# Optimization experiments

Hardware: AMD Instinct MI355X
Metric: run time of the kernel (lower is better)

Reference implementation:

```python
import jax, jax.numpy as jnp
import numpy as np

N_NODES = 10000
N_EDGES = 160000
MUL_N = 64    # node-feature multiplicity per irrep (0e and 1o)
MUL_F = 16    # field-feature multiplicity per irrep
SQ3 = np.sqrt(3.0).astype(np.float32)
SILU_GAIN = np.float32(1.679177)  # e3nn normalize2mom gain for silu


def split_irreps(x, mul):
    # x: [n, mul + 3*mul] laid out e3nn-style: scalars then vectors
    return x[:, :mul], x[:, mul:].reshape(x.shape[0], mul, 3)


def irrep_linear(s, v, Ws, Wv):
    # o3.Linear on (mul x0e + mul x1o): per-irrep channel mixing, 1/sqrt(fan_in)
    inv = np.float32(1.0 / np.sqrt(Ws.shape[0]))
    return (s @ Ws) * inv, jnp.einsum('nui,uv->nvi', v, Wv) * inv


def setup_inputs() -> dict:
    key = jax.random.key(0)
    ks = jax.random.split(key, 30)
    f32 = jnp.float32
    rn = lambda k, sh: jax.random.normal(k, sh, dtype=f32)
    inp = {
        'node_attrs': rn(ks[0], (N_NODES, 10)),
        'node_feats': rn(ks[1], (N_NODES, MUL_N + 3 * MUL_N)),
        'edge_attrs': rn(ks[2], (N_EDGES, 4)),
        'edge_feats': rn(ks[3], (N_EDGES, 8)),
        'field_feats': rn(ks[4], (N_NODES, MUL_F + 3 * MUL_F)),
        'edge_index': jax.random.randint(ks[5], (2, N_EDGES), 0, N_NODES, dtype=jnp.int32),
        # o3.Linear weights (linear1, linear2)
        'W1s': rn(ks[6], (MUL_N, MUL_N)), 'W1v': rn(ks[7], (MUL_N, MUL_N)),
        'W2s': rn(ks[8], (MUL_N, MUL_N)), 'W2v': rn(ks[9], (MUL_N, MUL_N)),
        # FullyConnectedNet [8,64,64,64,256]
        'mlp_w1': rn(ks[10], (8, 64)), 'mlp_w2': rn(ks[11], (64, 64)),
        'mlp_w3': rn(ks[12], (64, 64)), 'mlp_w4': rn(ks[13], (64, 4 * MUL_N)),
        # linear_v_sender / linear_v_receiver: 128x0e+128x1o -> 16x0e+16x1o
        'Wvs_s': rn(ks[14], (2 * MUL_N, MUL_F)), 'Wvs_v': rn(ks[15], (2 * MUL_N, MUL_F)),
        'Wvr_s': rn(ks[16], (2 * MUL_N, MUL_F)), 'Wvr_v': rn(ks[17], (2 * MUL_N, MUL_F)),
        # final FC tensor products (field x field -> 1x0e)
        'Wfs0': rn(ks[18], (MUL_F, MUL_F)), 'Wfs1': rn(ks[19], (MUL_F, MUL_F)),
        'Wfr0': rn(ks[20], (MUL_F, MUL_F)), 'Wfr1': rn(ks[21], (MUL_F, MUL_F)),
        # LinearInFieldChargesBlock FC TP: node x field -> 1x0e+1x1o
        'Wmp_ss': rn(ks[22], (MUL_N, MUL_F)), 'Wmp_vv': rn(ks[23], (MUL_N, MUL_F)),
        'Wmp_sv': rn(ks[24], (MUL_N, MUL_F)), 'Wmp_vs': rn(ks[25], (MUL_N, MUL_F)),
    }
    return inp


def reference(node_attrs, node_feats, edge_attrs, edge_feats, field_feats,
              W1s, W1v, W2s, W2v, mlp_w1, mlp_w2, mlp_w3, mlp_w4,
              Wvs_s, Wvs_v, Wvr_s, Wvr_v, Wfs0, Wfs1, Wfr0, Wfr1,
              Wmp_ss, Wmp_vv, Wmp_sv, Wmp_vs, edge_index):
    sender, receiver = edge_index[0], edge_index[1]
    num_nodes = node_feats.shape[0]

    # conv_tp weight MLP (e3nn FullyConnectedNet)
    h = edge_feats
    for W in (mlp_w1, mlp_w2, mlp_w3):
        h = jax.nn.silu((h @ W) * np.float32(1.0 / np.sqrt(W.shape[0]))) * SILU_GAIN
    tp_w = (h @ mlp_w4) * np.float32(1.0 / np.sqrt(mlp_w4.shape[0]))  # [E, 4*MUL_N]
    w = tp_w.reshape(-1, 4, MUL_N)

    ns, nv = split_irreps(node_feats, MUL_N)
    l1s, l1v = irrep_linear(ns, nv, W1s, W1v)
    l2s, l2v = irrep_linear(ns, nv, W2s, W2v)
    bs = l1s[sender] + l2s[receiver]   # [E, MUL_N]
    bv = l1v[sender] + l2v[receiver]   # [E, MUL_N, 3]

    y0 = edge_attrs[:, 0:1]            # [E,1] 0e harmonic
    y1 = edge_attrs[:, 1:4]            # [E,3] 1o harmonic
    # uvu CG tensor product with per-edge weights
    m00 = w[:, 0] * bs * y0                                          # 0e x 0e -> 0e
    m11 = w[:, 1] * jnp.einsum('eui,ei->eu', bv, y1) / SQ3           # 1o x 1o -> 0e
    m01 = w[:, 2][:, :, None] * bs[:, :, None] * y1[:, None, :]      # 0e x 1o -> 1o
    m10 = w[:, 3][:, :, None] * bv * y0[:, :, None]                  # 1o x 0e -> 1o
    ms = jnp.concatenate([m00, m11], axis=1)    # [E, 128]
    mv = jnp.concatenate([m01, m10], axis=1)    # [E, 128, 3]

    As, Av = irrep_linear(ms, mv, Wvs_s, Wvs_v)
    Bs, Bv = irrep_linear(ms, mv, Wvr_s, Wvr_v)

    fs, fv = split_irreps(field_feats, MUL_F)
    alpha = np.float32(1.0 / np.sqrt(2 * MUL_F * MUL_F))
    p_s = (jnp.einsum('eu,ev,uv->e', As, fs[sender], Wfs0)
           + jnp.einsum('eui,evi,uv->e', Av, fv[sender], Wfs1) / SQ3) * alpha
    p_r = (jnp.einsum('eu,ev,uv->e', Bs, fs[receiver], Wfr0)
           + jnp.einsum('eui,evi,uv->e', Bv, fv[receiver], Wfr1) / SQ3) * alpha
    p_ji = np.float32(0.1) * (p_s + p_r)   # [E]

    charges = (jax.ops.segment_sum(p_ji, receiver, num_segments=num_nodes)
               - jax.ops.segment_sum(p_ji, sender, num_segments=num_nodes))

    # field-dependent multipoles (FC TP, zero_charges=True then charge slot overwritten)
    a2 = np.float32(1.0 / np.sqrt(2 * MUL_N * MUL_F))
    mp0 = (jnp.einsum('nu,nv,uv->n', ns, fs, Wmp_ss)
           + jnp.einsum('nui,nvi,uv->n', nv, fv, Wmp_vv) / SQ3) * a2
    mp1 = (jnp.einsum('nu,nvi,uv->ni', ns, fv, Wmp_sv)
           + jnp.einsum('nui,nv,uv->ni', nv, fs, Wmp_vs)) * a2
    mpoles = np.float32(0.01) * jnp.concatenate([mp0[:, None], mp1], axis=1)  # [N,4]
    mpoles = mpoles.at[:, 0].set(charges)
    return mpoles[:, None, :], p_ji[:, None]
```

## Files before the change

### kernel.cpp

```cpp
#include <hip/hip_runtime.h>

#define NN 10000
#define NE 160000

#define INV8   0.35355339059327373f
#define QINV   0.125f
#define GAIN   1.679177f
#define ISQ3   0.57735026918962576f
#define FINALS 4.8828125e-5f
#define MPSC   2.2097086912079612e-4f

typedef __attribute__((ext_vector_type(8))) short bf16x8;
typedef __attribute__((ext_vector_type(4))) float f32x4;

__device__ __forceinline__ float4 ld4(const float* p){ return *(const float4*)p; }
__device__ __forceinline__ float sil(float x){ return x*GAIN/(1.f+__expf(-x)); }
__device__ __forceinline__ unsigned short f2b(float f){
  unsigned u = __float_as_uint(f);
  return (unsigned short)((u + 0x7FFFu + ((u>>16)&1u)) >> 16);
}
__device__ __forceinline__ float b2f(unsigned short b){
  return __uint_as_float(((unsigned)b) << 16);
}
__device__ __forceinline__ void st4b(unsigned short* p, float a, float b, float c, float d){
  unsigned long long v = (unsigned long long)f2b(a)
                       | ((unsigned long long)f2b(b) << 16)
                       | ((unsigned long long)f2b(c) << 32)
                       | ((unsigned long long)f2b(d) << 48);
  *(unsigned long long*)p = v;
}
__device__ __forceinline__ void up8(const unsigned short* p, float* f){
  const uint4 v = *(const uint4*)p;
  f[0]=__uint_as_float(v.x<<16); f[1]=__uint_as_float(v.x&0xFFFF0000u);
  f[2]=__uint_as_float(v.y<<16); f[3]=__uint_as_float(v.y&0xFFFF0000u);
  f[4]=__uint_as_float(v.z<<16); f[5]=__uint_as_float(v.z&0xFFFF0000u);
  f[6]=__uint_as_float(v.w<<16); f[7]=__uint_as_float(v.w&0xFFFF0000u);
}
#define C4(v,i) (((const float*)&(v))[i])

#define WQ_STRIDE 260
__global__ __launch_bounds__(256, 2) void edge_fused_kernel(
    const float* __restrict__ efe,
    const float* __restrict__ mw1, const float* __restrict__ mw2,
    const float* __restrict__ mw3, const float* __restrict__ mw4,
    const float* __restrict__ ea, const int* __restrict__ eidx,
    const unsigned short* __restrict__ wsS, const unsigned short* __restrict__ wsR,
    float* __restrict__ out)
{
  __shared__ __align__(16) unsigned char pool[8192 + 128*WQ_STRIDE*2];
  unsigned short* W4q = (unsigned short*)pool;
  unsigned short* W1t = (unsigned short*)(pool + 8192);
  unsigned short* W2t = (unsigned short*)(pool + 12288);
  unsigned short* W3t = (unsigned short*)(pool + 20480);
  unsigned short* H   = (unsigned short*)(pool + 28672);
  unsigned short* WQ  = (unsigned short*)(pool + 8192);

  const int tid = threadIdx.x;
  const int wv  = tid >> 6;
  const int l   = tid & 63;
  const int eb  = blockIdx.x * 128;

  #pragma unroll
  for (int it = 0; it < 16; ++it) {
    const int i = tid + 256*it, e = i >> 5, k = i & 31;
    H[e*64 + (k ^ ((e&7)<<3))] = (k < 8) ? f2b(efe[(size_t)(eb+e)*8 + k]) : 0;
  }
  #pragma unroll
  for (int it = 0; it < 8; ++it) {
    const int i = tid + 256*it, n = i >> 5, k = i & 31;
    W1t[n*32 + (k ^ ((n&3)<<3))] = (k < 8) ? f2b(mw1[k*64 + n]) : 0;
  }
  #pragma unroll
  for (int it = 0; it < 16; ++it) {
    const int i = tid + 256*it, k = i >> 6, n = i & 63;
    W2t[n*64 + (k ^ ((n&7)<<3))] = f2b(mw2[k*64 + n]);
    W3t[n*64 + (k ^ ((n&7)<<3))] = f2b(mw3[k*64 + n]);
  }
  __syncthreads();

  const int arow = l & 15;
  const int koff = (l >> 4) * 8;

  {
    bf16x8 a[8];
    #pragma unroll
    for (int mf = 0; mf < 8; ++mf) {
      const int e = mf*16 + arow;
      a[mf] = *(const bf16x8*)&H[e*64 + (koff ^ ((e&7)<<3))];
    }
    const int n = wv*16 + arow;
    const bf16x8 b = *(const bf16x8*)&W1t[n*32 + (koff ^ ((n&3)<<3))];
    __syncthreads();
    f32x4 acc[8];
    #pragma unroll
    for (int mf = 0; mf < 8; ++mf) {
      acc[mf] = (f32x4){0.f,0.f,0.f,0.f};
      acc[mf] = __builtin_amdgcn_mfma_f32_16x16x32_bf16(a[mf], b, acc[mf], 0, 0, 0);
    }
    #pragma unroll
    for (int mf = 0; mf < 8; ++mf)
      #pragma unroll
      for (int rg = 0; rg < 4; ++rg) {
        const int e = mf*16 + (l>>4)*4 + rg, j = wv*16 + arow;
        H[e*64 + (j ^ ((e&7)<<3))] = f2b(sil(acc[mf][rg]*INV8));
      }
    __syncthreads();
  }

  const unsigned short* Wt[2] = { W2t, W3t };
  #pragma unroll
  for (int ly = 0; ly < 2; ++ly) {
    bf16x8 a[16];
    #pragma unroll
    for (int mf = 0; mf < 8; ++mf)
      #pragma unroll
      for (int ks = 0; ks < 2; ++ks) {
        const int e = mf*16 + arow, kb = ks*32 + koff;
        a[mf*2+ks] = *(const bf16x8*)&H[e*64 + (kb ^ ((e&7)<<3))];
      }
    const int n = wv*16 + arow;
    bf16x8 b0, b1;
    {
      const int kb0 = koff, kb1 = 32 + koff;
      b0 = *(const bf16x8*)&Wt[ly][n*64 + (kb0 ^ ((n&7)<<3))];
      b1 = *(const bf16x8*)&Wt[ly][n*64 + (kb1 ^ ((n&7)<<3))];
    }
    __syncthreads();
    f32x4 acc[8];
    #pragma unroll
    for (int mf = 0; mf < 8; ++mf) {
      acc[mf] = (f32x4){0.f,0.f,0.f,0.f};
      acc[mf] = __builtin_amdgcn_mfma_f32_16x16x32_bf16(a[mf*2+0], b0, acc[mf], 0, 0, 0);
      acc[mf] = __builtin_amdgcn_mfma_f32_16x16x32_bf16(a[mf*2+1], b1, acc[mf], 0, 0, 0);
    }
    #pragma unroll
    for (int mf = 0; mf < 8; ++mf)
      #pragma unroll
      for (int rg = 0; rg < 4; ++rg) {
        const int e = mf*16 + (l>>4)*4 + rg, j = wv*16 + arow;
        H[e*64 + (j ^ ((e&7)<<3))] = f2b(sil(acc[mf][rg]*QINV));
      }
    __syncthreads();
  }

  bf16x8 a4[16];
  #pragma unroll
  for (int mf = 0; mf < 8; ++mf)
    #pragma unroll
    for (int ks = 0; ks < 2; ++ks) {
      const int e = mf*16 + arow, kb = ks*32 + koff;
      a4[mf*2+ks] = *(const bf16x8*)&H[e*64 + (kb ^ ((e&7)<<3))];
    }

  for (int q = 0; q < 4; ++q) {
    #pragma unroll
    for (int it = 0; it < 16; ++it) {
      const int i = tid + 256*it, k = i >> 6, nn = i & 63;
      W4q[nn*64 + (k ^ ((nn&7)<<3))] = f2b(mw4[k*256 + q*64 + nn]);
    }
    __syncthreads();

    const int n = wv*16 + arow;
    const bf16x8 b0 = *(const bf16x8*)&W4q[n*64 + ((koff     ) ^ ((n&7)<<3))];
    const bf16x8 b1 = *(const bf16x8*)&W4q[n*64 + ((32 + koff) ^ ((n&7)<<3))];
    f32x4 acc[8];
    #pragma unroll
    for (int mf = 0; mf < 8; ++mf) {
      acc[mf] = (f32x4){0.f,0.f,0.f,0.f};
      acc[mf] = __builtin_amdgcn_mfma_f32_16x16x32_bf16(a4[mf*2+0], b0, acc[mf], 0, 0, 0);
      acc[mf] = __builtin_amdgcn_mfma_f32_16x16x32_bf16(a4[mf*2+1], b1, acc[mf], 0, 0, 0);
    }
    #pragma unroll
    for (int mf = 0; mf < 8; ++mf)
      #pragma unroll
      for (int rg = 0; rg < 4; ++rg) {
        const int e = mf*16 + (l>>4)*4 + rg;
        const int j = q*64 + wv*16 + arow;
        WQ[e*WQ_STRIDE + j] = f2b(acc[mf][rg]);
      }
    __syncthreads();
  }

  {
    const int el  = tid >> 1;
    const int sub = tid & 1;
    const int e   = eb + el;
    const int s = eidx[e];
    const int r = eidx[NE + e];
    const float4 y = ld4(ea + (size_t)e*4);

    float accS = 0.f, accR = 0.f;
    const unsigned short* Sb = wsS + (size_t)s*768 + sub*384;
    const unsigned short* Rb = wsR + (size_t)r*768 + sub*384;
    const unsigned short* wrow = WQ + el*WQ_STRIDE;
    #pragma unroll 2
    for (int t = 0; t < 8; ++t) {
      const int uq = sub*8 + t;
      const unsigned short* Sr = Sb + t*48;
      const unsigned short* Rr = Rb + t*48;
      float S[48], R[48];
      up8(Sr+ 0, S+ 0); up8(Sr+ 8, S+ 8); up8(Sr+16, S+16);
      up8(Sr+24, S+24); up8(Sr+32, S+32); up8(Sr+40, S+40);
      up8(Rr+ 0, R+ 0); up8(Rr+ 8, R+ 8); up8(Rr+16, R+16);
      up8(Rr+24, R+24); up8(Rr+32, R+32); up8(Rr+40, R+40);

      float wq[16];
      #pragma unroll
      for (int m = 0; m < 4; ++m) {
        const unsigned long long v = *(const unsigned long long*)(wrow + m*64 + uq*4);
        #pragma unroll
        for (int d = 0; d < 4; ++d)
          wq[m*4+d] = b2f((unsigned short)(v >> (16*d)));
      }

      #pragma unroll
      for (int d = 0; d < 4; ++d) {
        const float bs = S[d]    + R[d];
        const float b0 = S[4+d]  + R[4+d];
        const float b1 = S[8+d]  + R[8+d];
        const float b2 = S[12+d] + R[12+d];
        const float bvy = b0*y.y + b1*y.z + b2*y.w;
        const float m0 = wq[d]    * bs * y.x;
        const float m1 = wq[4+d]  * bvy;
        const float m2 = wq[8+d]  * bs;
        const float m3 = wq[12+d] * y.x;
        accS += m0*S[16+d] + m1*S[20+d]
              + m2*(y.y*S[24+d] + y.z*S[28+d] + y.w*S[32+d])
              + m3*(b0*S[36+d] + b1*S[40+d] + b2*S[44+d]);
        accR += m0*R[16+d] + m1*R[20+d]
              + m2*(y.y*R[24+d] + y.z*R[28+d] + y.w*R[32+d])
              + m3*(b0*R[36+d] + b1*R[40+d] + b2*R[44+d]);
      }
    }
    float acc = FINALS * (accS + accR);
    acc += __shfl_xor(acc, 1, 64);
    if (sub == 0) {
      out[NN*4 + e] = acc;
      atomicAdd(out + (size_t)r*4, acc);
      atomicAdd(out + (size_t)s*4, -acc);
    }
  }
}

__global__ __launch_bounds__(256) void node_kernel(
    const float* __restrict__ nf, const float* __restrict__ ff,
    const float* __restrict__ W1s, const float* __restrict__ W1v,
    const float* __restrict__ W2s, const float* __restrict__ W2v,
    const float* __restrict__ Wvss, const float* __restrict__ Wvsv,
    const float* __restrict__ Wvrs, const float* __restrict__ Wvrv,
    const float* __restrict__ Wfs0, const float* __restrict__ Wfs1,
    const float* __restrict__ Wfr0, const float* __restrict__ Wfr1,
    const float* __restrict__ Wmsv, const float* __restrict__ Wmvs,
    unsigned short* __restrict__ wsS, unsigned short* __restrict__ wsR,
    float* __restrict__ out)
{
  const int lane = threadIdx.x & 63;
  const int Wid  = blockIdx.x * 4 + (threadIdx.x >> 6);
  const int p    = __builtin_amdgcn_readfirstlane(Wid & 7);
  const int grp  = __builtin_amdgcn_readfirstlane(Wid >> 3);
  const int n = grp * 64 + lane;
  if (n >= NN) return;
  const float* nrow = nf + (size_t)n * 256;
  const int vb = p * 8;
  const size_t rec = (size_t)n * 768;

  float a1s[8], a2s[8], a1v[3][8], a2v[3][8], t1[16];
  #pragma unroll
  for (int j = 0; j < 8; ++j){ a1s[j]=0.f; a2s[j]=0.f;
    a1v[0][j]=0.f; a1v[1][j]=0.f; a1v[2][j]=0.f;
    a2v[0][j]=0.f; a2v[1][j]=0.f; a2v[2][j]=0.f; }
  #pragma unroll
  for (int j = 0; j < 16; ++j) t1[j]=0.f;

  for (int u = 0; u < 64; ++u) {
    const float su  = nrow[u];
    const float nv0 = nrow[64+u*3+0];
    const float nv1 = nrow[64+u*3+1];
    const float nv2 = nrow[64+u*3+2];
    const float4 s1a = ld4(W1s+u*64+vb), s1b = ld4(W1s+u*64+vb+4);
    const float4 s2a = ld4(W2s+u*64+vb), s2b = ld4(W2s+u*64+vb+4);
    const float4 v1a = ld4(W1v+u*64+vb), v1b = ld4(W1v+u*64+vb+4);
    const float4 v2a = ld4(W2v+u*64+vb), v2b = ld4(W2v+u*64+vb+4);
    #pragma unroll
    for (int d = 0; d < 4; ++d) {
      a1s[d]     += su*C4(s1a,d);  a1s[4+d]     += su*C4(s1b,d);
      a2s[d]     += su*C4(s2a,d);  a2s[4+d]     += su*C4(s2b,d);
      a1v[0][d]  += nv0*C4(v1a,d); a1v[0][4+d]  += nv0*C4(v1b,d);
      a1v[1][d]  += nv1*C4(v1a,d); a1v[1][4+d]  += nv1*C4(v1b,d);
      a1v[2][d]  += nv2*C4(v1a,d); a1v[2][4+d]  += nv2*C4(v1b,d);
      a2v[0][d]  += nv0*C4(v2a,d); a2v[0][4+d]  += nv0*C4(v2b,d);
      a2v[1][d]  += nv1*C4(v2a,d); a2v[1][4+d]  += nv1*C4(v2b,d);
      a2v[2][d]  += nv2*C4(v2a,d); a2v[2][4+d]  += nv2*C4(v2b,d);
    }
    if (p == 0) {
      #pragma unroll
      for (int q = 0; q < 4; ++q) {
        const float4 m = ld4(Wmsv + u*16 + q*4);
        t1[q*4]   += su*m.x; t1[q*4+1] += su*m.y;
        t1[q*4+2] += su*m.z; t1[q*4+3] += su*m.w;
      }
    }
  }
  #pragma unroll
  for (int hh = 0; hh < 2; ++hh) {
    const int uq = 2*p + hh, o = hh*4;
    unsigned short* S = wsS + rec + uq*48;
    unsigned short* R = wsR + rec + uq*48;
    st4b(S+0,  a1s[o]*QINV, a1s[o+1]*QINV, a1s[o+2]*QINV, a1s[o+3]*QINV);
    st4b(S+4,  a1v[0][o]*QINV, a1v[0][o+1]*QINV, a1v[0][o+2]*QINV, a1v[0][o+3]*QINV);
    st4b(S+8,  a1v[1][o]*QINV, a1v[1][o+1]*QINV, a1v[1][o+2]*QINV, a1v[1][o+3]*QINV);
    st4b(S+12, a1v[2][o]*QINV, a1v[2][o+1]*QINV, a1v[2][o+2]*QINV, a1v[2][o+3]*QINV);
    st4b(R+0,  a2s[o]*QINV, a2s[o+1]*QINV, a2s[o+2]*QINV, a2s[o+3]*QINV);
    st4b(R+4,  a2v[0][o]*QINV, a2v[0][o+1]*QINV, a2v[0][o+2]*QINV, a2v[0][o+3]*QINV);
    st4b(R+8,  a2v[1][o]*QINV, a2v[1][o+1]*QINV, a2v[1][o+2]*QINV, a2v[1][o+3]*QINV);
    st4b(R+12, a2v[2][o]*QINV, a2v[2][o+1]*QINV, a2v[2][o+2]*QINV, a2v[2][o+3]*QINV);
  }

  float fsv[16], fvv[48];
  {
    const float* fr = ff + (size_t)n*64;
    #pragma unroll
    for (int q = 0; q < 4; ++q) {
      const float4 t = ld4(fr + q*4);
      fsv[q*4]=t.x; fsv[q*4+1]=t.y; fsv[q*4+2]=t.z; fsv[q*4+3]=t.w;
    }
    #pragma unroll
    for (int q = 0; q < 12; ++q) {
      const float4 t = ld4(fr + 16 + q*4);
      fvv[q*4]=t.x; fvv[q*4+1]=t.y; fvv[q*4+2]=t.z; fvv[q*4+3]=t.w;
    }
  }

  if (p == 0) {
    float m0=0.f, m1=0.f, m2=0.f;
    #pragma unroll
    for (int v = 0; v < 16; ++v) {
      m0 += t1[v]*fvv[v*3]; m1 += t1[v]*fvv[v*3+1]; m2 += t1[v]*fvv[v*3+2];
    }
    for (int u = 0; u < 64; ++u) {
      float t2 = 0.f;
      #pragma unroll
      for (int q = 0; q < 4; ++q) {
        const float4 w = ld4(Wmvs + u*16 + q*4);
        t2 += w.x*fsv[q*4] + w.y*fsv[q*4+1] + w.z*fsv[q*4+2] + w.w*fsv[q*4+3];
      }
      m0 += nrow[64+u*3+0]*t2;
      m1 += nrow[64+u*3+1]*t2;
      m2 += nrow[64+u*3+2]*t2;
    }
    float* o = out + (size_t)n*4;
    o[0] = 0.f;
    o[1] = MPSC*m0; o[2] = MPSC*m1; o[3] = MPSC*m2;
  }

  float gsA[16], gsB[16], gvA[48], gvB[48];
  #pragma unroll
  for (int up = 0; up < 16; ++up) {
    float sA=0.f,sB=0.f,vA0=0.f,vA1=0.f,vA2=0.f,vB0=0.f,vB1=0.f,vB2=0.f;
    #pragma unroll
    for (int q = 0; q < 4; ++q) {
      const float4 w0 = ld4(Wfs0 + up*16 + q*4);
      const float4 w1 = ld4(Wfs1 + up*16 + q*4);
      const float4 w2 = ld4(Wfr0 + up*16 + q*4);
      const float4 w3 = ld4(Wfr1 + up*16 + q*4);
      #pragma unroll
      for (int d = 0; d < 4; ++d) {
        const int v = q*4+d;
        sA  += C4(w0,d)*fsv[v];
        sB  += C4(w2,d)*fsv[v];
        vA0 += C4(w1,d)*fvv[v*3]; vA1 += C4(w1,d)*fvv[v*3+1]; vA2 += C4(w1,d)*fvv[v*3+2];
        vB0 += C4(w3,d)*fvv[v*3]; vB1 += C4(w3,d)*fvv[v*3+1]; vB2 += C4(w3,d)*fvv[v*3+2];
      }
    }
    gsA[up]=sA; gsB[up]=sB;
    gvA[up*3]=vA0; gvA[up*3+1]=vA1; gvA[up*3+2]=vA2;
    gvB[up*3]=vB0; gvB[up*3+1]=vB1; gvB[up*3+2]=vB2;
  }

  #pragma unroll
  for (int tq = 0; tq < 4; ++tq) {
    float qa[4], qb[4], ra[3][4], rb[3][4];
    #pragma unroll
    for (int d = 0; d < 4; ++d) {
      const int U = p*16 + tq*4 + d;
      float aq=0.f,bq=0.f,a0=0.f,a1=0.f,a2=0.f,b0=0.f,b1=0.f,b2=0.f;
      #pragma unroll
      for (int q = 0; q < 4; ++q) {
        const float4 ws_ = ld4(Wvss + U*16 + q*4);
        const float4 wr_ = ld4(Wvrs + U*16 + q*4);
        const float4 wv_ = ld4(Wvsv + U*16 + q*4);
        const float4 wu_ = ld4(Wvrv + U*16 + q*4);
        #pragma unroll
        for (int dd = 0; dd < 4; ++dd) {
          const int up = q*4+dd;
          aq += C4(ws_,dd)*gsA[up];
          bq += C4(wr_,dd)*gsB[up];
          a0 += C4(wv_,dd)*gvA[up*3]; a1 += C4(wv_,dd)*gvA[up*3+1]; a2 += C4(wv_,dd)*gvA[up*3+2];
          b0 += C4(wu_,dd)*gvB[up*3]; b1 += C4(wu_,dd)*gvB[up*3+1]; b2 += C4(wu_,dd)*gvB[up*3+2];
        }
      }
      qa[d]=aq; qb[d]=bq;
      ra[0][d]=a0*ISQ3; ra[1][d]=a1*ISQ3; ra[2][d]=a2*ISQ3;
      rb[0][d]=b0*ISQ3; rb[1][d]=b1*ISQ3; rb[2][d]=b2*ISQ3;
    }
    if (p < 4) {
      const int uq = p*4 + tq;
      unsigned short* S = wsS + rec + uq*48;
      unsigned short* R = wsR + rec + uq*48;
      st4b(S+16, qa[0],qa[1],qa[2],qa[3]);
      st4b(S+24, ra[0][0],ra[0][1],ra[0][2],ra[0][3]);
      st4b(S+28, ra[1][0],ra[1][1],ra[1][2],ra[1][3]);
      st4b(S+32, ra[2][0],ra[2][1],ra[2][2],ra[2][3]);
      st4b(R+16, qb[0],qb[1],qb[2],qb[3]);
      st4b(R+24, rb[0][0],rb[0][1],rb[0][2],rb[0][3]);
      st4b(R+28, rb[1][0],rb[1][1],rb[1][2],rb[1][3]);
      st4b(R+32, rb[2][0],rb[2][1],rb[2][2],rb[2][3]);
    } else {
      const int uq = (p-4)*4 + tq;
      unsigned short* S = wsS + rec + uq*48;
      unsigned short* R = wsR + rec + uq*48;
      st4b(S+20, qa[0]*ISQ3,qa[1]*ISQ3,qa[2]*ISQ3,qa[3]*ISQ3);
      st4b(S+36, ra[0][0],ra[0][1],ra[0][2],ra[0][3]);
      st4b(S+40, ra[1][0],ra[1][1],ra[1][2],ra[1][3]);
      st4b(S+44, ra[2][0],ra[2][1],ra[2][2],ra[2][3]);
      st4b(R+20, qb[0]*ISQ3,qb[1]*ISQ3,qb[2]*ISQ3,qb[3]*ISQ3);
      st4b(R+36, rb[0][0],rb[0][1],rb[0][2],rb[0][3]);
      st4b(R+40, rb[1][0],rb[1][1],rb[1][2],rb[1][3]);
      st4b(R+44, rb[2][0],rb[2][1],rb[2][2],rb[2][3]);
    }
  }
}

extern "C" void kernel_launch(void* const* d_in, const int* in_sizes, int n_in,
                              void* d_out, int out_size, void* d_ws, size_t ws_size,
                              hipStream_t stream) {
  (void)in_sizes; (void)n_in; (void)out_size; (void)ws_size;
  const float* node_feats  = (const float*)d_in[1];
  const float* edge_attrs  = (const float*)d_in[2];
  const float* edge_feats  = (const float*)d_in[3];
  const float* field_feats = (const float*)d_in[4];
  const int*   edge_index  = (const int*)  d_in[5];
  const float* W1s  = (const float*)d_in[6];
  const float* W1v  = (const float*)d_in[7];
  const float* W2s  = (const float*)d_in[8];
  const float* W2v  = (const float*)d_in[9];
  const float* mw1  = (const float*)d_in[10];
  const float* mw2  = (const float*)d_in[11];
  const float* mw3  = (const float*)d_in[12];
  const float* mw4  = (const float*)d_in[13];
  const float* Wvss = (const float*)d_in[14];
  const float* Wvsv = (const float*)d_in[15];
  const float* Wvrs = (const float*)d_in[16];
  const float* Wvrv = (const float*)d_in[17];
  const float* Wfs0 = (const float*)d_in[18];
  const float* Wfs1 = (const float*)d_in[19];
  const float* Wfr0 = (const float*)d_in[20];
  const float* Wfr1 = (const float*)d_in[21];
  const float* Wmsv = (const float*)d_in[24];
  const float* Wmvs = (const float*)d_in[25];

  float* out = (float*)d_out;
  unsigned short* wsS = (unsigned short*)d_ws;
  unsigned short* wsR = wsS + (size_t)NN*768;

  hipLaunchKernelGGL(node_kernel, dim3(314), dim3(256), 0, stream,
      node_feats, field_feats, W1s, W1v, W2s, W2v, Wvss, Wvsv, Wvrs, Wvrv,
      Wfs0, Wfs1, Wfr0, Wfr1, Wmsv, Wmvs, wsS, wsR, out);
  hipLaunchKernelGGL(edge_fused_kernel, dim3(NE/128), dim3(256), 0, stream,
      edge_feats, mw1, mw2, mw3, mw4, edge_attrs, edge_index, wsS, wsR, out);
}
```

Measured before the change: 215.9 us.

## Sort edges by receiver via counting sort before the fused edge kernel

```diff
diff --git a/kernel.cpp b/kernel.cpp
--- a/kernel.cpp
+++ b/kernel.cpp
@@ -38,12 +38,66 @@
 }
 #define C4(v,i) (((const float*)&(v))[i])
 
+__global__ __launch_bounds__(256) void sort_zero(unsigned* __restrict__ hist){
+  hist[blockIdx.x*256 + threadIdx.x] = 0u;
+}
+__global__ __launch_bounds__(256) void sort_hist(const int* __restrict__ eidx,
+                                                 unsigned* __restrict__ hist){
+  const int e = blockIdx.x*256 + threadIdx.x;
+  atomicAdd(&hist[eidx[NE + e]], 1u);
+}
+__global__ __launch_bounds__(256) void sort_scan(const unsigned* __restrict__ hist,
+                                                 unsigned* __restrict__ offs){
+  __shared__ unsigned part[256];
+  __shared__ unsigned base[256];
+  const int t = threadIdx.x;
+  unsigned s = 0;
+  #pragma unroll
+  for (int i = 0; i < 40; ++i) s += hist[t*40 + i];
+  part[t] = s;
+  __syncthreads();
+  if (t == 0) {
+    unsigned run = 0;
+    for (int i = 0; i < 256; ++i) { base[i] = run; run += part[i]; }
+  }
+  __syncthreads();
+  unsigned run = base[t];
+  #pragma unroll
+  for (int i = 0; i < 40; ++i) { offs[t*40 + i] = run; run += hist[t*40 + i]; }
+}
+__global__ __launch_bounds__(256) void sort_scatter(const int* __restrict__ eidx,
+                                                    unsigned* __restrict__ offs,
+                                                    unsigned* __restrict__ sorted){
+  const int e = blockIdx.x*256 + threadIdx.x;
+  const unsigned pos = atomicAdd(&offs[eidx[NE + e]], 1u);
+  sorted[pos] = (unsigned)e;
+}
+__global__ __launch_bounds__(256) void permute_kernel(
+    const unsigned* __restrict__ sorted,
+    const float* __restrict__ efe, const float* __restrict__ ea,
+    const int* __restrict__ eidx,
+    float* __restrict__ pefe, float* __restrict__ pea,
+    int* __restrict__ psr, int* __restrict__ peid)
+{
+  const int i = blockIdx.x*256 + threadIdx.x;
+  const int e = (int)sorted[i];
+  const float4 a = ld4(efe + (size_t)e*8);
+  const float4 b = ld4(efe + (size_t)e*8 + 4);
+  *(float4*)(pefe + (size_t)i*8)     = a;
+  *(float4*)(pefe + (size_t)i*8 + 4) = b;
+  *(float4*)(pea  + (size_t)i*4)     = ld4(ea + (size_t)e*4);
+  psr[i]      = eidx[e];
+  psr[NE + i] = eidx[NE + e];
+  peid[i]     = e;
+}
+
 #define WQ_STRIDE 260
 __global__ __launch_bounds__(256, 2) void edge_fused_kernel(
     const float* __restrict__ efe,
     const float* __restrict__ mw1, const float* __restrict__ mw2,
     const float* __restrict__ mw3, const float* __restrict__ mw4,
     const float* __restrict__ ea, const int* __restrict__ eidx,
+    const int* __restrict__ peid,
     const unsigned short* __restrict__ wsS, const unsigned short* __restrict__ wsR,
     float* __restrict__ out)
 {
@@ -235,7 +289,7 @@
     float acc = FINALS * (accS + accR);
     acc += __shfl_xor(acc, 1, 64);
     if (sub == 0) {
-      out[NN*4 + e] = acc;
+      out[NN*4 + peid[e]] = acc;
       atomicAdd(out + (size_t)r*4, acc);
       atomicAdd(out + (size_t)s*4, -acc);
     }
@@ -462,10 +516,24 @@
   float* out = (float*)d_out;
   unsigned short* wsS = (unsigned short*)d_ws;
   unsigned short* wsR = wsS + (size_t)NN*768;
+  float* pefe   = (float*)(wsR + (size_t)NN*768);
+  float* pea    = pefe + (size_t)NE*8;
+  int*   psr    = (int*)(pea + (size_t)NE*4);
+  int*   peid   = psr + (size_t)2*NE;
+  unsigned* hist   = (unsigned*)(peid + NE);
+  unsigned* offs   = hist + 10240;
+  unsigned* sorted = offs + 10240;
+
+  hipLaunchKernelGGL(sort_zero,    dim3(40),  dim3(256), 0, stream, hist);
+  hipLaunchKernelGGL(sort_hist,    dim3(625), dim3(256), 0, stream, edge_index, hist);
+  hipLaunchKernelGGL(sort_scan,    dim3(1),   dim3(256), 0, stream, hist, offs);
+  hipLaunchKernelGGL(sort_scatter, dim3(625), dim3(256), 0, stream, edge_index, offs, sorted);
+  hipLaunchKernelGGL(permute_kernel, dim3(625), dim3(256), 0, stream,
+      sorted, edge_feats, edge_attrs, edge_index, pefe, pea, psr, peid);
 
   hipLaunchKernelGGL(node_kernel, dim3(314), dim3(256), 0, stream,
       node_feats, field_feats, W1s, W1v, W2s, W2v, Wvss, Wvsv, Wvrs, Wvrv,
       Wfs0, Wfs1, Wfr0, Wfr1, Wmsv, Wmvs, wsS, wsR, out);
   hipLaunchKernelGGL(edge_fused_kernel, dim3(NE/128), dim3(256), 0, stream,
-      edge_feats, mw1, mw2, mw3, mw4, edge_attrs, edge_index, wsS, wsR, out);
-}
+      pefe, mw1, mw2, mw3, mw4, pea, psr, peid, wsS, wsR, out);
+}
```

Result: slower. 231.4 us (+7.2%).
